# Kernel optimization log

Measured on AMD Instinct MI355X. Metric: run time of the kernel, lower is better.

## Reference

```python
import jax, jax.numpy as jnp
import numpy as np

B, T, D, H, FA = 512, 64, 128, 128, 64


def setup_inputs() -> dict:
    key = jax.random.key(0)
    ks = jax.random.split(key, 14)
    n = lambda k, s: jax.random.normal(k, s, dtype=jnp.float32) * 0.05
    return {
        "X": jax.random.normal(ks[0], (B, T, D), dtype=jnp.float32),
        "attri_data": jax.random.normal(ks[1], (D, FA), dtype=jnp.float32),
        "w_attr1": n(ks[2], (FA, FA // 2)), "b_attr1": n(ks[3], (FA // 2,)),
        "w_attr2": n(ks[4], (FA // 2, 1)), "b_attr2": n(ks[5], (1,)),
        "w_a1": n(ks[6], (2 * H + T, H)), "b_a1": n(ks[7], (H,)),
        "w_a2": n(ks[8], (H, 1)), "b_a2": n(ks[9], (1,)),
        "w_ih": n(ks[10], (4 * H, D)), "w_hh": n(ks[11], (4 * H, H)),
        "b_ih": n(ks[12], (4 * H,)), "b_hh": n(ks[13], (4 * H,)),
    }


def reference(X, attri_data, w_attr1, b_attr1, w_attr2, b_attr2,
              w_a1, b_a1, w_a2, b_a2, w_ih, w_hh, b_ih, b_hh):
    b, t_dim, d = X.shape
    h_dim = w_hh.shape[1]

    # Attribute attention: softmax over the data_dim axis (dim=0)
    a = attri_data @ w_attr1 + b_attr1
    a = jnp.where(a > 0, a, 0.5 * a)  # LeakyReLU(negative_slope=0.5)
    alpha_attri = jax.nn.softmax(a @ w_attr2 + b_attr2, axis=0)  # [D, 1]
    X_attri = X * alpha_attri.reshape(1, 1, d)  # [B, T, D]
    Xp = jnp.transpose(X_attri, (0, 2, 1))      # [B, D, T] per-variable series

    def step(carry, x_t):  # x_t: [B, D]
        h, c = carry  # [B, H] each; state BEFORE consuming x_t (matches torch loop)
        feat = jnp.concatenate([
            jnp.broadcast_to(h[:, None, :], (b, d, h_dim)),
            jnp.broadcast_to(c[:, None, :], (b, d, h_dim)),
            Xp,
        ], axis=2)  # [B, D, 2H+T]
        e = jnp.tanh(feat @ w_a1 + b_a1) @ w_a2 + b_a2  # [B, D, 1]
        alpha_s = jax.nn.softmax(e[..., 0], axis=1)      # softmax over D
        x_tilde_t = alpha_s * x_t                        # [B, D]
        # LSTM cell (PyTorch gate order i, f, g, o)
        gates = x_t @ w_ih.T + b_ih + h @ w_hh.T + b_hh  # [B, 4H]
        i_g, f_g, g_g, o_g = jnp.split(gates, 4, axis=1)
        c_new = jax.nn.sigmoid(f_g) * c + jax.nn.sigmoid(i_g) * jnp.tanh(g_g)
        h_new = jax.nn.sigmoid(o_g) * jnp.tanh(c_new)
        return (h_new, c_new), x_tilde_t

    h0 = jnp.zeros((b, h_dim), X.dtype)
    c0 = jnp.zeros((b, h_dim), X.dtype)
    _, X_tilde = jax.lax.scan(step, (h0, c0), jnp.transpose(X_attri, (1, 0, 2)))
    return jnp.transpose(X_tilde, (1, 0, 2))  # [B, T, D]
```

## Files before the change

### kernel.cpp

```cpp
#include <hip/hip_runtime.h>
#include <hip/hip_bf16.h>
#include <cstddef>
#include <cstdint>

#define DEVI __device__ __forceinline__

typedef float f32x4 __attribute__((ext_vector_type(4)));
typedef __bf16 bf16x8 __attribute__((ext_vector_type(8)));

DEVI float fast_rcp(float x) { return __builtin_amdgcn_rcpf(x); }
DEVI float sigmoid_fast(float x) { return fast_rcp(1.0f + __expf(-x)); }
DEVI float tanh_fast(float x) { return 1.0f - 2.0f * fast_rcp(__expf(2.0f * x) + 1.0f); }
DEVI float4 ld4(const float* p) { return *reinterpret_cast<const float4*>(p); }
DEVI void st4(float* p, float4 v) { *reinterpret_cast<float4*>(p) = v; }
DEVI float f4c(const float4& v, int i) { return i == 0 ? v.x : i == 1 ? v.y : i == 2 ? v.z : v.w; }
DEVI unsigned short bfbits(float f) { return __builtin_bit_cast(unsigned short, (__bf16)f); }
DEVI unsigned pack2(float a, float b) {
  return (unsigned)bfbits(a) | ((unsigned)bfbits(b) << 16);
}
DEVI f32x4 cvt4(uint2 u) {
  f32x4 r;
  r[0] = __builtin_bit_cast(float, (u.x & 0xffffu) << 16);
  r[1] = __builtin_bit_cast(float, u.x & 0xffff0000u);
  r[2] = __builtin_bit_cast(float, (u.y & 0xffffu) << 16);
  r[3] = __builtin_bit_cast(float, u.y & 0xffff0000u);
  return r;
}
DEVI void barrier_lgkm() {
  __builtin_amdgcn_sched_barrier(0);
  asm volatile("s_waitcnt lgkmcnt(0)" ::: "memory");
  __builtin_amdgcn_s_barrier();
  __builtin_amdgcn_sched_barrier(0);
}

__global__ __launch_bounds__(256) void k_prep(
    const float* __restrict__ AD, const float* __restrict__ W1,
    const float* __restrict__ B1, const float* __restrict__ W2,
    const float* __restrict__ B2, const float* __restrict__ w_ih,
    const float* __restrict__ b_ih, const float* __restrict__ b_hh,
    const float* __restrict__ w_a1, float* __restrict__ alpha_g,
    __hip_bfloat16* __restrict__ wA, float* __restrict__ biasJ,
    __hip_bfloat16* __restrict__ w1T) {
  __shared__ float sh[64 * 132];
  int bid = blockIdx.x, tid = threadIdx.x;
  if (bid < 64) {
    float* sW1 = sh;
    float* sW2 = sh + 2048;
    float* sB1 = sh + 2080;
    float* red = sh + 2112;
    float* sA  = sh + 2240;
    float* sMS = sh + 2368;
    for (int i = tid; i < 2048; i += 256) sW1[i] = W1[i];
    if (tid < 32) { sW2[tid] = W2[tid]; sB1[tid] = B1[tid]; }
    __syncthreads();
    if (tid < 128) {
      float ad[64];
      #pragma unroll
      for (int f = 0; f < 64; ++f) ad[f] = AD[tid * 64 + f];
      float logit = B2[0];
      #pragma unroll
      for (int j = 0; j < 32; ++j) {
        float a = sB1[j];
        #pragma unroll
        for (int f = 0; f < 64; ++f) a = fmaf(ad[f], sW1[f * 32 + j], a);
        a = a > 0.0f ? a : 0.5f * a;
        logit = fmaf(a, sW2[j], logit);
      }
      red[tid] = logit;
    }
    __syncthreads();
    if (tid == 0) {
      float mx = red[0];
      for (int i = 1; i < 128; ++i) mx = fmaxf(mx, red[i]);
      float sm = 0.0f;
      for (int i = 0; i < 128; ++i) sm += __expf(red[i] - mx);
      sMS[0] = mx; sMS[1] = sm;
    }
    __syncthreads();
    if (tid < 128) {
      float a = __expf(red[tid] - sMS[0]) / sMS[1];
      sA[tid] = a;
      if (bid == 0) alpha_g[tid] = a;
    }
    __syncthreads();
    int i4 = bid * 256 + tid;
    int j = i4 >> 5, d0 = (i4 & 31) * 4;
    float4 w = ld4(&w_ih[(size_t)j * 128 + d0]);
    uint2 o;
    o.x = pack2(w.x * sA[d0], w.y * sA[d0 + 1]);
    o.y = pack2(w.z * sA[d0 + 2], w.w * sA[d0 + 3]);
    *reinterpret_cast<uint2*>(&wA[(size_t)j * 128 + d0]) = o;
    if (i4 < 128) {
      int jb = i4 * 4;
      float4 v0 = ld4(&b_ih[jb]), v1 = ld4(&b_hh[jb]);
      v0.x += v1.x; v0.y += v1.y; v0.z += v1.z; v0.w += v1.w;
      st4(&biasJ[jb], v0);
    }
  } else {
    float (*tile)[132] = reinterpret_cast<float(*)[132]>(sh);
    int blk = bid - 64;
    #pragma unroll
    for (int i = 0; i < 32; ++i) {
      int idx = i * 256 + tid;
      int r = idx >> 7, c = idx & 127;
      tile[r][c] = w_a1[(size_t)(blk * 64 + r) * 128 + c];
    }
    __syncthreads();
    int n = tid >> 1, mh = tid & 1;
    unsigned* dst = reinterpret_cast<unsigned*>(&w1T[(size_t)n * 256 + blk * 64 + mh * 32]);
    #pragma unroll
    for (int i = 0; i < 16; ++i) {
      float a = tile[mh * 32 + 2 * i][n];
      float b = tile[mh * 32 + 2 * i + 1][n];
      dst[i] = pack2(a, b);
    }
  }
}

__global__ __launch_bounds__(256, 2) void k_gxw(
    const float* __restrict__ X, const __hip_bfloat16* __restrict__ wA,
    const float* __restrict__ biasJ, __hip_bfloat16* __restrict__ gx) {
  int rt = blockIdx.x, jt = blockIdx.y;
  int tid = threadIdx.x;
  int wv = tid >> 6, l = tid & 63, lg = l >> 4, lr = l & 15;
  int r0 = rt * 128;
  int j0 = jt * 128 + wv * 32;

  bf16x8 a[2][4];
  #pragma unroll
  for (int ri = 0; ri < 2; ++ri)
    #pragma unroll
    for (int ks = 0; ks < 4; ++ks)
      a[ri][ks] = *reinterpret_cast<const bf16x8*>(
          &wA[(size_t)(j0 + ri * 16 + lr) * 128 + ks * 32 + lg * 8]);

  f32x4 acc[2][8];
  #pragma unroll
  for (int ri = 0; ri < 2; ++ri)
    #pragma unroll
    for (int nj = 0; nj < 8; ++nj) acc[ri][nj] = (f32x4){0.f, 0.f, 0.f, 0.f};

  #pragma unroll 2
  for (int nj = 0; nj < 8; ++nj) {
    bf16x8 bh[4];
    #pragma unroll
    for (int ks = 0; ks < 4; ++ks) {
      const float* src = &X[(size_t)(r0 + nj * 16 + lr) * 128 + ks * 32 + lg * 8];
      float4 f0 = ld4(src), f1 = ld4(src + 4);
      bf16x8 fr;
      fr[0] = (__bf16)f0.x; fr[1] = (__bf16)f0.y;
      fr[2] = (__bf16)f0.z; fr[3] = (__bf16)f0.w;
      fr[4] = (__bf16)f1.x; fr[5] = (__bf16)f1.y;
      fr[6] = (__bf16)f1.z; fr[7] = (__bf16)f1.w;
      bh[ks] = fr;
    }
    #pragma unroll
    for (int ks = 0; ks < 4; ++ks) {
      acc[0][nj] = __builtin_amdgcn_mfma_f32_16x16x32_bf16(a[0][ks], bh[ks], acc[0][nj], 0, 0, 0);
      acc[1][nj] = __builtin_amdgcn_mfma_f32_16x16x32_bf16(a[1][ks], bh[ks], acc[1][nj], 0, 0, 0);
    }
  }

  #pragma unroll
  for (int ri = 0; ri < 2; ++ri) {
    int jb = j0 + ri * 16 + lg * 4;
    float4 bi = ld4(&biasJ[jb]);
    #pragma unroll
    for (int nj = 0; nj < 8; ++nj) {
      int row = r0 + nj * 16 + lr;
      uint2 o;
      o.x = pack2(acc[ri][nj][0] + bi.x, acc[ri][nj][1] + bi.y);
      o.y = pack2(acc[ri][nj][2] + bi.z, acc[ri][nj][3] + bi.w);
      *reinterpret_cast<uint2*>(&gx[(size_t)row * 512 + jb]) = o;
    }
  }
}

__global__ __launch_bounds__(512, 1) void k_recep(
    const __hip_bfloat16* __restrict__ gx, const float* __restrict__ w_hh,
    const __hip_bfloat16* __restrict__ w1T, float* __restrict__ EQ,
    const float* __restrict__ X, const float* __restrict__ w_a1,
    const float* __restrict__ b_a1, const float* __restrict__ alpha_g,
    float* __restrict__ EP) {
  __shared__ float shmem[2 * 64 * 128];
  int bid = blockIdx.x;
  int tid = threadIdx.x;

  if (bid >= 32) {
    int b = bid - 32;
    float (*Xb)[128] = reinterpret_cast<float(*)[128]>(&shmem[0]);
    float (*Wx)[128] = reinterpret_cast<float(*)[128]>(&shmem[8192]);
    #pragma unroll
    for (int i = 0; i < 4; ++i) {
      int l4 = i * 512 + tid;
      int r = l4 >> 5, c4 = l4 & 31;
      st4(&Xb[r][c4 * 4], ld4(&X[((size_t)b * 64 + r) * 128 + c4 * 4]));
      st4(&Wx[r][c4 * 4], ld4(&w_a1[(size_t)(256 + r) * 128 + c4 * 4]));
    }
    __syncthreads();
    int dg = tid & 15, kg = tid >> 4;
    float acc[8][4] = {};
    #pragma unroll 4
    for (int tau = 0; tau < 64; ++tau) {
      float4 xa0 = ld4(&Xb[tau][dg * 4]);
      float4 xa1 = ld4(&Xb[tau][64 + dg * 4]);
      float4 wa = ld4(&Wx[tau][kg * 4]);
      #pragma unroll
      for (int i = 0; i < 8; ++i) {
        float xv = (i < 4) ? f4c(xa0, i) : f4c(xa1, i - 4);
        #pragma unroll
        for (int j = 0; j < 4; ++j)
          acc[i][j] = fmaf(xv, f4c(wa, j), acc[i][j]);
      }
    }
    float4 ba = ld4(&b_a1[kg * 4]);
    #pragma unroll
    for (int i = 0; i < 8; ++i) {
      int drow = (i < 4) ? dg * 4 + i : 64 + dg * 4 + (i - 4);
      float al = alpha_g[drow];
      float4 o;
      float* po = &o.x;
      #pragma unroll
      for (int j = 0; j < 4; ++j) {
        float v = 2.0f * fmaf(al, acc[i][j], f4c(ba, j));
        po[j] = __expf(fminf(fmaxf(v, -40.0f), 40.0f));
      }
      st4(&EP[((size_t)b * 128 + drow) * 128 + kg * 4], o);
    }
    return;
  }

  unsigned short* kBp = reinterpret_cast<unsigned short*>(shmem);
  unsigned short* kCp = kBp + 4096;
  int wv = tid >> 6, l = tid & 63, lg = l >> 4, lr = l & 15;
  int b0 = bid * 16;

  bf16x8 ah[4][4];
  #pragma unroll
  for (int ks = 0; ks < 4; ++ks)
    #pragma unroll
    for (int q = 0; q < 4; ++q) {
      const float* src = &w_hh[(size_t)(q * 128 + wv * 16 + lr) * 128 + ks * 32 + lg * 8];
      float4 f0 = ld4(src), f1 = ld4(src + 4);
      bf16x8 fr;
      fr[0] = (__bf16)f0.x; fr[1] = (__bf16)f0.y;
      fr[2] = (__bf16)f0.z; fr[3] = (__bf16)f0.w;
      fr[4] = (__bf16)f1.x; fr[5] = (__bf16)f1.y;
      fr[6] = (__bf16)f1.z; fr[7] = (__bf16)f1.w;
      ah[ks][q] = fr;
    }

  bf16x8 wt[8];
  #pragma unroll
  for (int ks = 0; ks < 8; ++ks)
    wt[ks] = *reinterpret_cast<const bf16x8*>(
        &w1T[(size_t)(wv * 16 + lr) * 256 + ks * 32 + lg * 8]);

  alignas(16) float hA[4] = {0.f, 0.f, 0.f, 0.f};
  alignas(16) float cA[4] = {0.f, 0.f, 0.f, 0.f};
  int m0 = wv * 16 + lg * 4;
  int wIdx = lr * 128 + (((m0 >> 3) ^ lr) << 3) + (m0 & 7);
  const __hip_bfloat16* gxb = gx + (size_t)(b0 + lr) * 64 * 512 + wv * 16 + lg * 4;

  uint2 z; z.x = 0u; z.y = 0u;
  *reinterpret_cast<uint2*>(&kBp[wIdx]) = z;
  *reinterpret_cast<uint2*>(&kCp[wIdx]) = z;
  uint2 gA[4], gB[4];
  #pragma unroll
  for (int q = 0; q < 4; ++q) gA[q] = *reinterpret_cast<const uint2*>(gxb + q * 128);
  #pragma unroll
  for (int q = 0; q < 4; ++q) gB[q] = *reinterpret_cast<const uint2*>(gxb + 512 + q * 128);
  __syncthreads();

#define REC_STEP(T, SRC, DST, G)                                               \
  do {                                                                         \
    int t_ = (T);                                                              \
    bf16x8 bh[4], bc[4];                                                       \
    _Pragma("unroll")                                                          \
    for (int ks = 0; ks < 4; ++ks) {                                           \
      int idx_ = lr * 128 + ((((ks << 2) + lg) ^ lr) << 3);                    \
      bh[ks] = *reinterpret_cast<const bf16x8*>(&kBp[(SRC) * 2048 + idx_]);    \
      bc[ks] = *reinterpret_cast<const bf16x8*>(&kCp[(SRC) * 2048 + idx_]);    \
    }                                                                          \
    f32x4 ac0 = cvt4(G[0]), ac1 = cvt4(G[1]), ac2 = cvt4(G[2]), ac3 = cvt4(G[3]); \
    int tn_ = t_ + 2 < 64 ? t_ + 2 : 63;                                       \
    _Pragma("unroll")                                                          \
    for (int q = 0; q < 4; ++q)                                                \
      G[q] = *reinterpret_cast<const uint2*>(gxb + (size_t)tn_ * 512 + q * 128); \
    f32x4 ea = (f32x4){0.f, 0.f, 0.f, 0.f};                                    \
    _Pragma("unroll")                                                          \
    for (int ks = 0; ks < 4; ++ks) {                                           \
      ac0 = __builtin_amdgcn_mfma_f32_16x16x32_bf16(ah[ks][0], bh[ks], ac0, 0, 0, 0); \
      ac1 = __builtin_amdgcn_mfma_f32_16x16x32_bf16(ah[ks][1], bh[ks], ac1, 0, 0, 0); \
      ac2 = __builtin_amdgcn_mfma_f32_16x16x32_bf16(ah[ks][2], bh[ks], ac2, 0, 0, 0); \
      ac3 = __builtin_amdgcn_mfma_f32_16x16x32_bf16(ah[ks][3], bh[ks], ac3, 0, 0, 0); \
    }                                                                          \
    _Pragma("unroll")                                                          \
    for (int ks = 0; ks < 4; ++ks)                                             \
      ea = __builtin_amdgcn_mfma_f32_16x16x32_bf16(wt[ks], bh[ks], ea, 0, 0, 0); \
    _Pragma("unroll")                                                          \
    for (int ks = 0; ks < 4; ++ks)                                             \
      ea = __builtin_amdgcn_mfma_f32_16x16x32_bf16(wt[ks + 4], bc[ks], ea, 0, 0, 0); \
    {                                                                          \
      float4 eo;                                                               \
      float* pe = &eo.x;                                                       \
      _Pragma("unroll")                                                        \
      for (int r = 0; r < 4; ++r) {                                            \
        float v = 2.0f * ea[r];                                                \
        pe[r] = __expf(fminf(fmaxf(v, -40.0f), 40.0f));                        \
      }                                                                        \
      st4(&EQ[((size_t)(t_ * 512) + b0 + lr) * 128 + wv * 16 + lg * 4], eo);   \
    }                                                                          \
    _Pragma("unroll")                                                          \
    for (int r = 0; r < 4; ++r) {                                              \
      float ig = sigmoid_fast(ac0[r]);                                         \
      float fg = sigmoid_fast(ac1[r]);                                         \
      float gg = tanh_fast(ac2[r]);                                            \
      float og = sigmoid_fast(ac3[r]);                                         \
      float cn = fmaf(fg, cA[r], ig * gg);                                     \
      float hn = og * tanh_fast(cn);                                           \
      cA[r] = cn; hA[r] = hn;                                                  \
    }                                                                          \
    {                                                                          \
      uint2 hu; hu.x = pack2(hA[0], hA[1]); hu.y = pack2(hA[2], hA[3]);        \
      uint2 cu; cu.x = pack2(cA[0], cA[1]); cu.y = pack2(cA[2], cA[3]);        \
      *reinterpret_cast<uint2*>(&kBp[(DST) * 2048 + wIdx]) = hu;               \
      *reinterpret_cast<uint2*>(&kCp[(DST) * 2048 + wIdx]) = cu;               \
    }                                                                          \
    barrier_lgkm();                                                            \
  } while (0)

  #pragma unroll 1
  for (int it = 0; it < 32; ++it) {
    REC_STEP(2 * it, 0, 1, gA);
    REC_STEP(2 * it + 1, 1, 0, gB);
  }
#undef REC_STEP
}

__global__ __launch_bounds__(512, 2) void k_attn(
    const float* __restrict__ EP, const float* __restrict__ EQ,
    const float* __restrict__ w_a2, const float* __restrict__ alpha,
    const float* __restrict__ X, float* __restrict__ out) {
  __shared__ float EQs[64][128];
  __shared__ float e_lds[8][128];
  int b = blockIdx.x;
  int tid = threadIdx.x;
  #pragma unroll
  for (int i = 0; i < 4; ++i) {
    int l4 = i * 512 + tid;
    int t = l4 >> 5, k4 = l4 & 31;
    st4(&EQs[t][k4 * 4], ld4(&EQ[((size_t)t * 512 + b) * 128 + k4 * 4]));
  }
  int d = tid >> 2, s = tid & 3;
  float4 ep[8], w2r[8];
  #pragma unroll
  for (int q = 0; q < 8; ++q) {
    ep[q]  = ld4(&EP[((size_t)b * 128 + d) * 128 + s * 32 + q * 4]);
    w2r[q] = ld4(&w_a2[s * 32 + q * 4]);
  }
  int wv = tid >> 6, l = tid & 63;
  float al0 = alpha[l], al1 = alpha[64 + l];
  __syncthreads();

  for (int rnd = 0; rnd < 8; ++rnd) {
    #pragma unroll
    for (int it = 0; it < 8; ++it) {
      int t = rnd * 8 + it;
      float p = 0.0f;
      #pragma unroll
      for (int q = 0; q < 8; ++q) {
        float4 eq = ld4(&EQs[t][s * 32 + q * 4]);
        p = fmaf(w2r[q].x, fast_rcp(fmaf(ep[q].x, eq.x, 1.0f)), p);
        p = fmaf(w2r[q].y, fast_rcp(fmaf(ep[q].y, eq.y, 1.0f)), p);
        p = fmaf(w2r[q].z, fast_rcp(fmaf(ep[q].z, eq.z, 1.0f)), p);
        p = fmaf(w2r[q].w, fast_rcp(fmaf(ep[q].w, eq.w, 1.0f)), p);
      }
      p += __shfl_xor(p, 1);
      p += __shfl_xor(p, 2);
      if (s == 0) e_lds[it][d] = -2.0f * p;
    }
    __syncthreads();
    {
      int t = rnd * 8 + wv;
      float v0 = e_lds[wv][l], v1 = e_lds[wv][64 + l];
      float mx = fmaxf(v0, v1);
      #pragma unroll
      for (int o = 1; o < 64; o <<= 1) mx = fmaxf(mx, __shfl_xor(mx, o));
      float e0 = __expf(v0 - mx), e1 = __expf(v1 - mx);
      float sm = e0 + e1;
      #pragma unroll
      for (int o = 1; o < 64; o <<= 1) sm += __shfl_xor(sm, o);
      float inv = fast_rcp(sm);
      size_t ro = ((size_t)b * 64 + t) * 128;
      out[ro + l]      = e0 * inv * al0 * X[ro + l];
      out[ro + 64 + l] = e1 * inv * al1 * X[ro + 64 + l];
    }
    __syncthreads();
  }
}

extern "C" void kernel_launch(void* const* d_in, const int* in_sizes, int n_in,
                              void* d_out, int out_size, void* d_ws, size_t ws_size,
                              hipStream_t stream) {
  const float* X    = (const float*)d_in[0];
  const float* AD   = (const float*)d_in[1];
  const float* W1   = (const float*)d_in[2];
  const float* B1   = (const float*)d_in[3];
  const float* W2   = (const float*)d_in[4];
  const float* B2   = (const float*)d_in[5];
  const float* w_a1 = (const float*)d_in[6];
  const float* b_a1 = (const float*)d_in[7];
  const float* w_a2 = (const float*)d_in[8];
  const float* w_ih = (const float*)d_in[10];
  const float* w_hh = (const float*)d_in[11];
  const float* b_ih = (const float*)d_in[12];
  const float* b_hh = (const float*)d_in[13];
  float* out = (float*)d_out;
  float* ws = (float*)d_ws;

  float* alpha = ws;
  float* EQ    = ws + 256;
  float* EP    = EQ + 4194304;
  float* fgx   = EP + 8388608;
  __hip_bfloat16* gx = (__hip_bfloat16*)fgx;
  float* fw1T  = fgx + 8388608;
  __hip_bfloat16* w1T = (__hip_bfloat16*)fw1T;
  float* fwA   = fw1T + 16384;
  __hip_bfloat16* wA = (__hip_bfloat16*)fwA;
  float* biasJ = fwA + 32768;

  hipLaunchKernelGGL(k_prep,  dim3(68),      dim3(256), 0, stream,
                     AD, W1, B1, W2, B2, w_ih, b_ih, b_hh, w_a1,
                     alpha, wA, biasJ, w1T);
  hipLaunchKernelGGL(k_gxw,   dim3(256, 4),  dim3(256), 0, stream, X, wA, biasJ, gx);
  hipLaunchKernelGGL(k_recep, dim3(544),     dim3(512), 0, stream,
                     gx, w_hh, w1T, EQ, X, w_a1, b_a1, alpha, EP);
  hipLaunchKernelGGL(k_attn,  dim3(512),     dim3(512), 0, stream,
                     EP, EQ, w_a2, alpha, X, out);
}
```

Before: 331.0 us.

## Defer EQ projection off recurrent critical path and coalesce gx writes via LDS

In the recurrent kernel, the attention EQ projection for step t is now computed at the start of step t+1 from saved h/c fragments, so its MFMAs and exp/store overlap with the next step's work instead of lengthening each step before the barrier. The gate-input GEMM kernel stages its bf16 outputs through a shared-memory tile and writes full 16-byte row segments, and the grid is reordered. The attention kernel splits its dot-product accumulation into two independent chains for more ILP. Keeping the previous operands live adds register pressure in the recurrent kernel.

```diff
diff --git a/kernel.cpp b/kernel.cpp
--- a/kernel.cpp
+++ b/kernel.cpp
@@ -120,7 +120,8 @@
 __global__ __launch_bounds__(256, 2) void k_gxw(
     const float* __restrict__ X, const __hip_bfloat16* __restrict__ wA,
     const float* __restrict__ biasJ, __hip_bfloat16* __restrict__ gx) {
-  int rt = blockIdx.x, jt = blockIdx.y;
+  __shared__ unsigned short tile[128 * 136];
+  int jt = blockIdx.x, rt = blockIdx.y;
   int tid = threadIdx.x;
   int wv = tid >> 6, l = tid & 63, lg = l >> 4, lr = l & 15;
   int r0 = rt * 128;
@@ -165,14 +166,24 @@
   for (int ri = 0; ri < 2; ++ri) {
     int jb = j0 + ri * 16 + lg * 4;
     float4 bi = ld4(&biasJ[jb]);
+    int jloc = wv * 32 + ri * 16 + lg * 4;
     #pragma unroll
     for (int nj = 0; nj < 8; ++nj) {
-      int row = r0 + nj * 16 + lr;
+      int row = nj * 16 + lr;
       uint2 o;
       o.x = pack2(acc[ri][nj][0] + bi.x, acc[ri][nj][1] + bi.y);
       o.y = pack2(acc[ri][nj][2] + bi.z, acc[ri][nj][3] + bi.w);
-      *reinterpret_cast<uint2*>(&gx[(size_t)row * 512 + jb]) = o;
-    }
+      *reinterpret_cast<uint2*>(&tile[row * 136 + jloc]) = o;
+    }
+  }
+  __syncthreads();
+
+  #pragma unroll
+  for (int i = 0; i < 8; ++i) {
+    int idx = i * 256 + tid;
+    int row = idx >> 4, seg = idx & 15;
+    uint4 v = *reinterpret_cast<const uint4*>(&tile[row * 136 + seg * 8]);
+    *reinterpret_cast<uint4*>(&gx[(size_t)(r0 + row) * 512 + jt * 128 + seg * 8]) = v;
   }
 }
 
@@ -272,9 +283,31 @@
   for (int q = 0; q < 4; ++q) gB[q] = *reinterpret_cast<const uint2*>(gxb + 512 + q * 128);
   __syncthreads();
 
-#define REC_STEP(T, SRC, DST, G)                                               \
+  bf16x8 pbh[4], pbc[4];
+
+#define EQ_EMIT(PT)                                                            \
+  do {                                                                         \
+    f32x4 eh = (f32x4){0.f, 0.f, 0.f, 0.f};                                    \
+    f32x4 ec = (f32x4){0.f, 0.f, 0.f, 0.f};                                    \
+    _Pragma("unroll")                                                          \
+    for (int ks = 0; ks < 4; ++ks) {                                           \
+      eh = __builtin_amdgcn_mfma_f32_16x16x32_bf16(wt[ks], pbh[ks], eh, 0, 0, 0); \
+      ec = __builtin_amdgcn_mfma_f32_16x16x32_bf16(wt[ks + 4], pbc[ks], ec, 0, 0, 0); \
+    }                                                                          \
+    float4 eo;                                                                 \
+    float* pe = &eo.x;                                                         \
+    _Pragma("unroll")                                                          \
+    for (int r = 0; r < 4; ++r) {                                              \
+      float v = 2.0f * (eh[r] + ec[r]);                                        \
+      pe[r] = __expf(fminf(fmaxf(v, -40.0f), 40.0f));                          \
+    }                                                                          \
+    st4(&EQ[((size_t)((PT) * 512) + b0 + lr) * 128 + wv * 16 + lg * 4], eo);   \
+  } while (0)
+
+#define REC_STEP(T, SRC, DST, G, EMIT)                                         \
   do {                                                                         \
     int t_ = (T);                                                              \
+    if (EMIT) EQ_EMIT(t_ - 1);                                                 \
     bf16x8 bh[4], bc[4];                                                       \
     _Pragma("unroll")                                                          \
     for (int ks = 0; ks < 4; ++ks) {                                           \
@@ -287,29 +320,12 @@
     _Pragma("unroll")                                                          \
     for (int q = 0; q < 4; ++q)                                                \
       G[q] = *reinterpret_cast<const uint2*>(gxb + (size_t)tn_ * 512 + q * 128); \
-    f32x4 ea = (f32x4){0.f, 0.f, 0.f, 0.f};                                    \
     _Pragma("unroll")                                                          \
     for (int ks = 0; ks < 4; ++ks) {                                           \
       ac0 = __builtin_amdgcn_mfma_f32_16x16x32_bf16(ah[ks][0], bh[ks], ac0, 0, 0, 0); \
       ac1 = __builtin_amdgcn_mfma_f32_16x16x32_bf16(ah[ks][1], bh[ks], ac1, 0, 0, 0); \
       ac2 = __builtin_amdgcn_mfma_f32_16x16x32_bf16(ah[ks][2], bh[ks], ac2, 0, 0, 0); \
       ac3 = __builtin_amdgcn_mfma_f32_16x16x32_bf16(ah[ks][3], bh[ks], ac3, 0, 0, 0); \
-    }                                                                          \
-    _Pragma("unroll")                                                          \
-    for (int ks = 0; ks < 4; ++ks)                                             \
-      ea = __builtin_amdgcn_mfma_f32_16x16x32_bf16(wt[ks], bh[ks], ea, 0, 0, 0); \
-    _Pragma("unroll")                                                          \
-    for (int ks = 0; ks < 4; ++ks)                                             \
-      ea = __builtin_amdgcn_mfma_f32_16x16x32_bf16(wt[ks + 4], bc[ks], ea, 0, 0, 0); \
-    {                                                                          \
-      float4 eo;                                                               \
-      float* pe = &eo.x;                                                       \
-      _Pragma("unroll")                                                        \
-      for (int r = 0; r < 4; ++r) {                                            \
-        float v = 2.0f * ea[r];                                                \
-        pe[r] = __expf(fminf(fmaxf(v, -40.0f), 40.0f));                        \
-      }                                                                        \
-      st4(&EQ[((size_t)(t_ * 512) + b0 + lr) * 128 + wv * 16 + lg * 4], eo);   \
     }                                                                          \
     _Pragma("unroll")                                                          \
     for (int r = 0; r < 4; ++r) {                                              \
@@ -327,15 +343,21 @@
       *reinterpret_cast<uint2*>(&kBp[(DST) * 2048 + wIdx]) = hu;               \
       *reinterpret_cast<uint2*>(&kCp[(DST) * 2048 + wIdx]) = cu;               \
     }                                                                          \
+    _Pragma("unroll")                                                          \
+    for (int ks = 0; ks < 4; ++ks) { pbh[ks] = bh[ks]; pbc[ks] = bc[ks]; }     \
     barrier_lgkm();                                                            \
   } while (0)
 
+  REC_STEP(0, 0, 1, gA, 0);
+  REC_STEP(1, 1, 0, gB, 1);
   #pragma unroll 1
-  for (int it = 0; it < 32; ++it) {
-    REC_STEP(2 * it, 0, 1, gA);
-    REC_STEP(2 * it + 1, 1, 0, gB);
-  }
+  for (int it = 1; it < 32; ++it) {
+    REC_STEP(2 * it, 0, 1, gA, 1);
+    REC_STEP(2 * it + 1, 1, 0, gB, 1);
+  }
+  EQ_EMIT(63);
 #undef REC_STEP
+#undef EQ_EMIT
 }
 
 __global__ __launch_bounds__(512, 2) void k_attn(
@@ -367,15 +389,21 @@
     #pragma unroll
     for (int it = 0; it < 8; ++it) {
       int t = rnd * 8 + it;
-      float p = 0.0f;
-      #pragma unroll
-      for (int q = 0; q < 8; ++q) {
-        float4 eq = ld4(&EQs[t][s * 32 + q * 4]);
-        p = fmaf(w2r[q].x, fast_rcp(fmaf(ep[q].x, eq.x, 1.0f)), p);
-        p = fmaf(w2r[q].y, fast_rcp(fmaf(ep[q].y, eq.y, 1.0f)), p);
-        p = fmaf(w2r[q].z, fast_rcp(fmaf(ep[q].z, eq.z, 1.0f)), p);
-        p = fmaf(w2r[q].w, fast_rcp(fmaf(ep[q].w, eq.w, 1.0f)), p);
+      float pa = 0.0f, pb = 0.0f;
+      #pragma unroll
+      for (int q = 0; q < 4; ++q) {
+        float4 eqa = ld4(&EQs[t][s * 32 + q * 4]);
+        float4 eqb = ld4(&EQs[t][s * 32 + 16 + q * 4]);
+        pa = fmaf(w2r[q].x, fast_rcp(fmaf(ep[q].x, eqa.x, 1.0f)), pa);
+        pa = fmaf(w2r[q].y, fast_rcp(fmaf(ep[q].y, eqa.y, 1.0f)), pa);
+        pa = fmaf(w2r[q].z, fast_rcp(fmaf(ep[q].z, eqa.z, 1.0f)), pa);
+        pa = fmaf(w2r[q].w, fast_rcp(fmaf(ep[q].w, eqa.w, 1.0f)), pa);
+        pb = fmaf(w2r[q + 4].x, fast_rcp(fmaf(ep[q + 4].x, eqb.x, 1.0f)), pb);
+        pb = fmaf(w2r[q + 4].y, fast_rcp(fmaf(ep[q + 4].y, eqb.y, 1.0f)), pb);
+        pb = fmaf(w2r[q + 4].z, fast_rcp(fmaf(ep[q + 4].z, eqb.z, 1.0f)), pb);
+        pb = fmaf(w2r[q + 4].w, fast_rcp(fmaf(ep[q + 4].w, eqb.w, 1.0f)), pb);
       }
+      float p = pa + pb;
       p += __shfl_xor(p, 1);
       p += __shfl_xor(p, 2);
       if (s == 0) e_lds[it][d] = -2.0f * p;
@@ -433,7 +461,7 @@
   hipLaunchKernelGGL(k_prep,  dim3(68),      dim3(256), 0, stream,
                      AD, W1, B1, W2, B2, w_ih, b_ih, b_hh, w_a1,
                      alpha, wA, biasJ, w1T);
-  hipLaunchKernelGGL(k_gxw,   dim3(256, 4),  dim3(256), 0, stream, X, wA, biasJ, gx);
+  hipLaunchKernelGGL(k_gxw,   dim3(4, 256),  dim3(256), 0, stream, X, wA, biasJ, gx);
   hipLaunchKernelGGL(k_recep, dim3(544),     dim3(512), 0, stream,
                      gx, w_hh, w1T, EQ, X, w_a1, b_a1, alpha, EP);
   hipLaunchKernelGGL(k_attn,  dim3(512),     dim3(512), 0, stream,
```

After: 321.1 us. -3.0%, faster.
